# Kernel optimization log

Measured on AMD Instinct MI355X. Metric: run time of the kernel, lower is better.

Reference implementation:

```python
import jax, jax.numpy as jnp
import numpy as np

NEG_SLOPE = 0.2  # PyG GATConv default negative_slope
EPS = 1e-16


def gat_conv(x, src, dst, num_nodes, W, a_src, a_dst, bias, heads, out_c, concat):
    """PyG-style GATConv (eval mode, self-loops already appended).
    x: [N, F_in]; src/dst: [E] (edge j->i with src=j, dst=i).
    W: [F_in, heads*out_c]; a_src/a_dst: [heads, out_c]; bias: [heads*out_c] or [out_c].
    """
    xw = (x @ W).reshape(num_nodes, heads, out_c)          # [N, H, C]
    alpha_src = jnp.sum(xw * a_src, axis=-1)               # [N, H]
    alpha_dst = jnp.sum(xw * a_dst, axis=-1)               # [N, H]
    e = jax.nn.leaky_relu(alpha_src[src] + alpha_dst[dst], NEG_SLOPE)  # [E, H]
    # numerically stable segment softmax over edges grouped by destination node
    m = jax.ops.segment_max(e, dst, num_segments=num_nodes)            # [N, H]
    e = jnp.exp(e - m[dst])
    denom = jax.ops.segment_sum(e, dst, num_segments=num_nodes)        # [N, H]
    alpha = e / (denom[dst] + EPS)                                     # [E, H]
    # weighted scatter-sum aggregation of source messages
    out = jax.ops.segment_sum(xw[src] * alpha[:, :, None], dst, num_segments=num_nodes)  # [N, H, C]
    if concat:
        out = out.reshape(num_nodes, heads * out_c)
    else:
        out = out.mean(axis=1)
    return out + bias


def setup_inputs() -> dict:
    key = jax.random.key(0)
    ks = jax.random.split(key, 12)
    N, E = 50000, 800000
    F_in, Hid, H1, Out = 512, 32, 8, 64

    def xavier(k, shape, gain=1.414):
        fan_in, fan_out = shape[0], shape[-1] if len(shape) == 2 else int(np.prod(shape[1:]))
        a = gain * np.sqrt(6.0 / (fan_in + fan_out))
        return jax.random.uniform(k, shape, jnp.float32, -a, a)

    x = jax.random.normal(ks[0], (N, F_in), jnp.float32)
    edge_index = jax.random.randint(ks[1], (2, E), 0, N, jnp.int64)

    W1 = xavier(ks[2], (F_in, H1 * Hid))
    a_src1 = xavier(ks[3], (H1, Hid))
    a_dst1 = xavier(ks[4], (H1, Hid))
    b1 = jnp.zeros((H1 * Hid,), jnp.float32)

    W2 = xavier(ks[5], (H1 * Hid, Out))
    a_src2 = xavier(ks[6], (1, Out))
    a_dst2 = xavier(ks[7], (1, Out))
    b2 = jnp.zeros((Out,), jnp.float32)

    return {"x": x, "edge_index": edge_index,
            "W1": W1, "a_src1": a_src1, "a_dst1": a_dst1, "b1": b1,
            "W2": W2, "a_src2": a_src2, "a_dst2": a_dst2, "b2": b2}


def reference(x, edge_index, W1, a_src1, a_dst1, b1, W2, a_src2, a_dst2, b2):
    N = x.shape[0]
    # add self-loops (PyG GATConv default add_self_loops=True)
    loop = jnp.arange(N, dtype=edge_index.dtype)
    src = jnp.concatenate([edge_index[0], loop])
    dst = jnp.concatenate([edge_index[1], loop])

    # eval mode: all dropouts are identity
    h = gat_conv(x, src, dst, N, W1, a_src1, a_dst1, b1, heads=8, out_c=32, concat=True)
    h = jax.nn.elu(h)
    h = gat_conv(h, src, dst, N, W2, a_src2, a_dst2, b2, heads=1, out_c=64, concat=False)
    return jax.nn.log_softmax(h, axis=1)
```

## Files before the change

kernel.cpp:

```cpp
#include <hip/hip_runtime.h>
#include <hip/hip_bf16.h>


typedef __attribute__((ext_vector_type(8)))  __bf16          bf16x8;
typedef __attribute__((ext_vector_type(8)))  unsigned short  ushort8;
typedef __attribute__((ext_vector_type(16))) float           f32x16;

#define NEG_SLOPE 0.2f
#define EPS_GAT 1e-16f

static __device__ __forceinline__ float lrelu(float x) {
    return x > 0.0f ? x : NEG_SLOPE * x;
}
static __device__ __forceinline__ unsigned short f2bf(float f) {
    unsigned u = __float_as_uint(f);
    return (unsigned short)((u + 0x7fffu + ((u >> 16) & 1u)) >> 16);
}
static __device__ __forceinline__ float bf2f(unsigned short v) {
    return __uint_as_float(((unsigned)v) << 16);
}
static __device__ __forceinline__ unsigned encf(float x) {
    unsigned u = __float_as_uint(x);
    return (u >> 31) ? ~u : (u | 0x80000000u);
}
static __device__ __forceinline__ float decf(unsigned e) {
    unsigned u = (e >> 31) ? (e & 0x7fffffffu) : ~e;
    return __uint_as_float(u);
}

__global__ void k_hist_w(const void* __restrict__ eix, int* __restrict__ counts,
                         int E, int EB,
                         const float* __restrict__ W1, const float* __restrict__ W2,
                         unsigned short* __restrict__ w1t, unsigned short* __restrict__ w2t) {
    int b = blockIdx.x;
    if (b < EB) {
        int i = b * 256 + threadIdx.x;
        unsigned w = ((const unsigned*)eix)[2 * min(i, E - 1) + 1];
        bool is64 = (__syncthreads_or((int)(w != 0u)) == 0);
        if (i < E) {
            int d = is64 ? (int)((const long long*)eix)[E + i]
                         : ((const int*)eix)[E + i];
            atomicAdd(&counts[d], 1);
        }
    } else {
        int t = (b - EB) * 256 + threadIdx.x;
        if (t < 512 * 256) {
            int k = t >> 8, m = t & 255;
            w1t[m * 512 + k] = f2bf(W1[t]);
        } else {
            int u = t - 512 * 256;
            if (u < 256 * 64) {
                int k = u >> 6, m = u & 63;
                w2t[m * 256 + k] = f2bf(W2[u]);
            }
        }
    }
}

__global__ void k_scan1(const int* __restrict__ counts, int* __restrict__ rowp,
                        int* __restrict__ bsum, int N) {
    __shared__ int s[256];
    int t = threadIdx.x, i = blockIdx.x * 256 + t;
    int v = (i < N) ? counts[i] : 0;
    s[t] = v;
    __syncthreads();
    for (int off = 1; off < 256; off <<= 1) {
        int u = (t >= off) ? s[t - off] : 0;
        __syncthreads();
        s[t] += u;
        __syncthreads();
    }
    if (i < N) rowp[i] = s[t] - v;
    if (t == 255) bsum[blockIdx.x] = s[255];
}

__global__ void k_scan2(const int* __restrict__ bsum, int* __restrict__ boff,
                        int* __restrict__ rowp_last, int NB) {
    __shared__ int s[256];
    int t = threadIdx.x;
    int v = (t < NB) ? bsum[t] : 0;
    s[t] = v;
    __syncthreads();
    for (int off = 1; off < 256; off <<= 1) {
        int u = (t >= off) ? s[t - off] : 0;
        __syncthreads();
        s[t] += u;
        __syncthreads();
    }
    if (t < NB) boff[t] = s[t] - v;
    if (t == 255) *rowp_last = s[255];
}

__global__ void k_scan3(int* __restrict__ rowp, int* __restrict__ cursor,
                        const int* __restrict__ boff, int N) {
    int i = blockIdx.x * 256 + threadIdx.x;
    if (i < N) {
        int r = rowp[i] + boff[blockIdx.x];
        rowp[i] = r;
        cursor[i] = r;
    }
}

__global__ void k_fill(const void* __restrict__ eix, int* __restrict__ cursor,
                       int* __restrict__ ssrc, int E) {
    int i = blockIdx.x * 256 + threadIdx.x;
    unsigned w = ((const unsigned*)eix)[2 * min(i, E - 1) + 1];
    bool is64 = (__syncthreads_or((int)(w != 0u)) == 0);
    if (i >= E) return;
    int s, d;
    if (is64) {
        s = (int)((const long long*)eix)[i];
        d = (int)((const long long*)eix)[E + i];
    } else {
        s = ((const int*)eix)[i];
        d = ((const int*)eix)[E + i];
    }
    int pos = atomicAdd(&cursor[d], 1);
    ssrc[pos] = s;
}

template <int BM, int BN, int NT, bool AF32, bool OUTBF>
__global__ __launch_bounds__(NT) void k_gemm(const void* __restrict__ Ain,
                                             const unsigned short* __restrict__ Bt,
                                             void* __restrict__ Cout, int Nrows, int K) {
    constexpr int LD = 40;
    __shared__ __align__(16) unsigned short As[BM * LD];
    __shared__ __align__(16) unsigned short Bs[BN * LD];
    const int tid = threadIdx.x;
    const int blockRow = blockIdx.x * BM;
    const int wave = tid >> 6, lane = tid & 63;
    constexpr int WR = BM / 64;
    const int wr = wave % WR, wc = wave / WR;
    const int m = lane & 31;
    const int ksel = (lane >> 5) * 8;

    f32x16 acc00{}, acc01{}, acc10{}, acc11{};

    for (int kt = 0; kt < K; kt += 32) {
        if constexpr (AF32) {
            const float* A = (const float*)Ain;
            for (int idx = tid; idx < BM * 4; idx += NT) {
                int r = idx >> 2, kc = (idx & 3) * 8;
                int grow = blockRow + r;
                union { ushort8 u; __hip_bfloat162 h[4]; } cv;
                if (grow < Nrows) {
                    const float* ap = A + (size_t)grow * K + kt + kc;
                    float4 x0 = *(const float4*)ap;
                    float4 x1 = *(const float4*)(ap + 4);
                    cv.h[0] = __float22bfloat162_rn(make_float2(x0.x, x0.y));
                    cv.h[1] = __float22bfloat162_rn(make_float2(x0.z, x0.w));
                    cv.h[2] = __float22bfloat162_rn(make_float2(x1.x, x1.y));
                    cv.h[3] = __float22bfloat162_rn(make_float2(x1.z, x1.w));
                } else {
                    cv.u = ushort8{};
                }
                *(ushort8*)&As[r * LD + kc] = cv.u;
            }
        } else {
            const unsigned short* A = (const unsigned short*)Ain;
            for (int idx = tid; idx < BM * 4; idx += NT) {
                int r = idx >> 2, kc = (idx & 3) * 8;
                int grow = blockRow + r;
                ushort8 o{};
                if (grow < Nrows) o = *(const ushort8*)(A + (size_t)grow * K + kt + kc);
                *(ushort8*)&As[r * LD + kc] = o;
            }
        }
        for (int idx = tid; idx < BN * 4; idx += NT) {
            int r = idx >> 2, kc = (idx & 3) * 8;
            *(ushort8*)&Bs[r * LD + kc] = *(const ushort8*)(Bt + (size_t)r * K + kt + kc);
        }
        __syncthreads();

        #pragma unroll
        for (int kk = 0; kk < 32; kk += 16) {
            bf16x8 a0 = *(const bf16x8*)&As[(wr * 64 +      m) * LD + kk + ksel];
            bf16x8 a1 = *(const bf16x8*)&As[(wr * 64 + 32 + m) * LD + kk + ksel];
            bf16x8 b0 = *(const bf16x8*)&Bs[(wc * 64 +      m) * LD + kk + ksel];
            bf16x8 b1 = *(const bf16x8*)&Bs[(wc * 64 + 32 + m) * LD + kk + ksel];
            acc00 = __builtin_amdgcn_mfma_f32_32x32x16_bf16(a0, b0, acc00, 0, 0, 0);
            acc01 = __builtin_amdgcn_mfma_f32_32x32x16_bf16(a0, b1, acc01, 0, 0, 0);
            acc10 = __builtin_amdgcn_mfma_f32_32x32x16_bf16(a1, b0, acc10, 0, 0, 0);
            acc11 = __builtin_amdgcn_mfma_f32_32x32x16_bf16(a1, b1, acc11, 0, 0, 0);
        }
        __syncthreads();
    }

    const int dcol = wc * 64 + (lane & 31);
    const int dquad = 4 * (lane >> 5);
    auto store_tile = [&](const f32x16& a, int rt, int ct) {
        #pragma unroll
        for (int r = 0; r < 16; ++r) {
            int row = blockRow + wr * 64 + rt * 32 + (r & 3) + 8 * (r >> 2) + dquad;
            if (row < Nrows) {
                size_t off = (size_t)row * BN + dcol + ct * 32;
                if constexpr (OUTBF) ((unsigned short*)Cout)[off] = f2bf(a[r]);
                else                 ((float*)Cout)[off] = a[r];
            }
        }
    };
    store_tile(acc00, 0, 0); store_tile(acc01, 0, 1);
    store_tile(acc10, 1, 0); store_tile(acc11, 1, 1);
}

__global__ void k_alpha(const unsigned short* __restrict__ xw, const float* __restrict__ a_s,
                        const float* __restrict__ a_d, float* __restrict__ os,
                        float* __restrict__ od, unsigned* __restrict__ Menc,
                        int NH, int H, int C) {
    __shared__ float red[256];
    int t = blockIdx.x * 256 + threadIdx.x;
    float s = -1e30f, d = 0.f;
    if (t < NH) {
        int n = t / H, h = t - n * H;
        const unsigned short* row = xw + (size_t)n * H * C + h * C;
        s = 0.f;
        for (int c = 0; c < C; c += 8) {
            ushort8 v = *(const ushort8*)(row + c);
            #pragma unroll
            for (int q = 0; q < 8; ++q) {
                float f = bf2f(v[q]);
                s += f * a_s[h * C + c + q];
                d += f * a_d[h * C + c + q];
            }
        }
        os[t] = s; od[t] = d;
    }
    red[threadIdx.x] = s;
    __syncthreads();
    for (int off = 128; off >= H; off >>= 1) {
        if (threadIdx.x < off) red[threadIdx.x] = fmaxf(red[threadIdx.x], red[threadIdx.x + off]);
        __syncthreads();
    }
    if ((int)threadIdx.x < H) atomicMax(&Menc[threadIdx.x], encf(red[threadIdx.x]));
}

__global__ __launch_bounds__(256) void k_agg_l1(
        const unsigned short* __restrict__ xw1, const float* __restrict__ asrc,
        const float* __restrict__ adst, const unsigned* __restrict__ Menc,
        const float* __restrict__ b1, const int* __restrict__ rp,
        const int* __restrict__ ssrc, unsigned short* __restrict__ hbf, int N) {
    int wid = (blockIdx.x * 256 + threadIdx.x) >> 6;
    if (wid >= N) return;
    int lane = threadIdx.x & 63;
    int g  = lane >> 4;
    int q  = lane & 15;
    int f0 = q * 16;
    int h  = q >> 1;
    int ih = wid * 8 + h;
    float ad = adst[ih];
    float m  = lrelu(decf(Menc[h]) + ad);
    float acc[16];
    float s;
    {
        float w = (g == 0) ? __expf(lrelu(asrc[ih] + ad) - m) : 0.0f;
        const unsigned short* pr = xw1 + (size_t)wid * 256 + f0;
        ushort8 lo = *(const ushort8*)pr;
        ushort8 hi = *(const ushort8*)(pr + 8);
        s = w;
        #pragma unroll
        for (int i = 0; i < 8; ++i) { acc[i] = w * bf2f(lo[i]); acc[8 + i] = w * bf2f(hi[i]); }
    }
    int e0 = rp[wid], e1 = rp[wid + 1];
    if (e0 < e1) {
        int eA = e0;
        bool vA = eA + g < e1;
        int jA = ssrc[min(eA + g, e1 - 1)];
        float asA = asrc[jA * 8 + h];
        const unsigned short* pA = xw1 + (size_t)jA * 256 + f0;
        ushort8 loA = *(const ushort8*)pA;
        ushort8 hiA = *(const ushort8*)(pA + 8);
        int eB = e0 + 4;
        bool hasB = eB < e1;
        bool vB = false; int jB = 0;
        if (hasB) { vB = eB + g < e1; jB = ssrc[min(eB + g, e1 - 1)]; }
        int eC = e0 + 8;
        while (true) {
            bool hasC = eC < e1;
            bool vC = false; int jC = 0;
            if (hasC) { vC = eC + g < e1; jC = ssrc[min(eC + g, e1 - 1)]; }
            float asB = 0.f; ushort8 loB{}, hiB{};
            if (hasB) {
                asB = asrc[jB * 8 + h];
                const unsigned short* pB = xw1 + (size_t)jB * 256 + f0;
                loB = *(const ushort8*)pB;
                hiB = *(const ushort8*)(pB + 8);
            }
            float w = vA ? __expf(lrelu(asA + ad) - m) : 0.0f;
            s += w;
            #pragma unroll
            for (int i = 0; i < 8; ++i) {
                acc[i]     += w * bf2f(loA[i]);
                acc[8 + i] += w * bf2f(hiA[i]);
            }
            if (!hasB) break;
            vA = vB; asA = asB; loA = loB; hiA = hiB;
            jB = jC; vB = vC; hasB = hasC;
            eC += 4;
        }
    }
    s += __shfl_xor(s, 16, 64);
    s += __shfl_xor(s, 32, 64);
    #pragma unroll
    for (int i = 0; i < 16; ++i) {
        acc[i] += __shfl_xor(acc[i], 16, 64);
        acc[i] += __shfl_xor(acc[i], 32, 64);
    }
    float inv = 1.0f / (s + EPS_GAT);
    int fw = f0 + g * 4;
    ushort4 o;
    #pragma unroll
    for (int i = 0; i < 4; ++i) {
        float v = acc[g * 4 + i] * inv + b1[fw + i];
        v = v > 0.f ? v : expm1f(v);
        ((unsigned short*)&o)[i] = f2bf(v);
    }
    *(ushort4*)(hbf + (size_t)wid * 256 + fw) = o;
}

__global__ __launch_bounds__(256) void k_agg_l2(
        const unsigned short* __restrict__ xw2, const float* __restrict__ asrc,
        const float* __restrict__ adst, const unsigned* __restrict__ Menc,
        const float* __restrict__ b2, const int* __restrict__ rp,
        const int* __restrict__ ssrc, float* __restrict__ out, int N) {
    int wid = (blockIdx.x * 256 + threadIdx.x) >> 6;
    if (wid >= N) return;
    int lane = threadIdx.x & 63;
    int g  = lane >> 3;
    int q  = lane & 7;
    int f0 = q * 8;
    float ad = adst[wid];
    float m = lrelu(decf(Menc[0]) + ad);
    float acc[8];
    float s;
    {
        float w = (g == 0) ? __expf(lrelu(asrc[wid] + ad) - m) : 0.0f;
        ushort8 xv = *(const ushort8*)(xw2 + (size_t)wid * 64 + f0);
        s = w;
        #pragma unroll
        for (int i = 0; i < 8; ++i) acc[i] = w * bf2f(xv[i]);
    }
    int e0 = rp[wid], e1 = rp[wid + 1];
    if (e0 < e1) {
        int eA = e0;
        bool vA = eA + g < e1;
        int jA = ssrc[min(eA + g, e1 - 1)];
        float asA = asrc[jA];
        ushort8 xvA = *(const ushort8*)(xw2 + (size_t)jA * 64 + f0);
        int eB = e0 + 8;
        bool hasB = eB < e1;
        bool vB = false; int jB = 0;
        if (hasB) { vB = eB + g < e1; jB = ssrc[min(eB + g, e1 - 1)]; }
        int eC = e0 + 16;
        while (true) {
            bool hasC = eC < e1;
            bool vC = false; int jC = 0;
            if (hasC) { vC = eC + g < e1; jC = ssrc[min(eC + g, e1 - 1)]; }
            float asB = 0.f; ushort8 xvB{};
            if (hasB) {
                asB = asrc[jB];
                xvB = *(const ushort8*)(xw2 + (size_t)jB * 64 + f0);
            }
            float w = vA ? __expf(lrelu(asA + ad) - m) : 0.0f;
            s += w;
            #pragma unroll
            for (int i = 0; i < 8; ++i) acc[i] += w * bf2f(xvA[i]);
            if (!hasB) break;
            vA = vB; asA = asB; xvA = xvB;
            jB = jC; vB = vC; hasB = hasC;
            eC += 8;
        }
    }
    s += __shfl_xor(s, 8, 64);
    s += __shfl_xor(s, 16, 64);
    s += __shfl_xor(s, 32, 64);
    #pragma unroll
    for (int i = 0; i < 8; ++i) {
        acc[i] += __shfl_xor(acc[i], 8, 64);
        acc[i] += __shfl_xor(acc[i], 16, 64);
        acc[i] += __shfl_xor(acc[i], 32, 64);
    }
    float inv = 1.0f / (s + EPS_GAT);
    float val[8];
    float mx = -1e30f;
    #pragma unroll
    for (int i = 0; i < 8; ++i) {
        val[i] = acc[i] * inv + b2[f0 + i];
        mx = fmaxf(mx, val[i]);
    }
    #pragma unroll
    for (int off = 4; off > 0; off >>= 1) mx = fmaxf(mx, __shfl_xor(mx, off, 64));
    float sm = 0.f;
    #pragma unroll
    for (int i = 0; i < 8; ++i) sm += __expf(val[i] - mx);
    #pragma unroll
    for (int off = 4; off > 0; off >>= 1) sm += __shfl_xor(sm, off, 64);
    float lse = mx + logf(sm);
    if (g == 0) {
        float4 o0 = make_float4(val[0] - lse, val[1] - lse, val[2] - lse, val[3] - lse);
        float4 o1 = make_float4(val[4] - lse, val[5] - lse, val[6] - lse, val[7] - lse);
        *(float4*)(out + (size_t)wid * 64 + f0)     = o0;
        *(float4*)(out + (size_t)wid * 64 + f0 + 4) = o1;
    }
}

static inline int cdiv(int a, int b) { return (a + b - 1) / b; }

extern "C" void kernel_launch(void* const* d_in, const int* in_sizes, int n_in,
                              void* d_out, int out_size, void* d_ws, size_t ws_size,
                              hipStream_t stream) {
    const float* x   = (const float*)d_in[0];
    const void*  eix = d_in[1];
    const float* W1  = (const float*)d_in[2];
    const float* as1 = (const float*)d_in[3];
    const float* ad1 = (const float*)d_in[4];
    const float* b1  = (const float*)d_in[5];
    const float* W2  = (const float*)d_in[6];
    const float* as2 = (const float*)d_in[7];
    const float* ad2 = (const float*)d_in[8];
    const float* b2  = (const float*)d_in[9];
    float* out = (float*)d_out;

    const int N = in_sizes[0] / 512;
    const int E = in_sizes[1] / 2;
    const int EB = cdiv(E, 256);
    const int WB = cdiv(512 * 256 + 256 * 64, 256);
    const int NB = cdiv(N, 256);
    const int NB1 = cdiv(N * 8, 256);
    const int NB2 = cdiv(N, 256);
    (void)n_in; (void)out_size; (void)ws_size;

    char* base = (char*)d_ws;
    size_t o = 0;
    auto alloc = [&](size_t bytes) -> char* {
        o = (o + 255) & ~(size_t)255;
        char* p = base + o;
        o += bytes;
        return p;
    };
    unsigned short* xw1b  = (unsigned short*)alloc((size_t)N * 256 * 2);
    unsigned short* hbf   = (unsigned short*)alloc((size_t)N * 256 * 2);
    unsigned short* xw2b  = (unsigned short*)alloc((size_t)N * 64 * 2);
    float*          asrc1 = (float*)alloc((size_t)N * 8 * 4);
    float*          adst1 = (float*)alloc((size_t)N * 8 * 4);
    float*          asrc2 = (float*)alloc((size_t)N * 4);
    float*          adst2 = (float*)alloc((size_t)N * 4);
    size_t zero_begin = (o + 255) & ~(size_t)255;
    unsigned*       Menc  = (unsigned*)alloc(16 * 4);
    int*            counts= (int*)alloc((size_t)N * 4);
    size_t zero_end = o;
    int*            cursor= (int*)alloc((size_t)N * 4);
    int*            rowp  = (int*)alloc((size_t)(N + 1) * 4);
    int*            bsum  = (int*)alloc(256 * 4);
    int*            boff  = (int*)alloc(256 * 4);
    unsigned short* w1t   = (unsigned short*)alloc(512 * 256 * 2);
    unsigned short* w2t   = (unsigned short*)alloc(256 * 64 * 2);
    int*            ssrc  = (int*)alloc((size_t)E * 4);

    hipMemsetAsync(base + zero_begin, 0, zero_end - zero_begin, stream);

    k_hist_w<<<EB + WB, 256, 0, stream>>>(eix, counts, E, EB, W1, W2, w1t, w2t);
    k_scan1<<<NB, 256, 0, stream>>>(counts, rowp, bsum, N);
    k_scan2<<<1, 256, 0, stream>>>(bsum, boff, rowp + N, NB);
    k_scan3<<<NB, 256, 0, stream>>>(rowp, cursor, boff, N);
    k_fill<<<EB, 256, 0, stream>>>(eix, cursor, ssrc, E);

    k_gemm<128, 256, 512, true, true><<<cdiv(N, 128), 512, 0, stream>>>(x, w1t, xw1b, N, 512);
    k_alpha<<<NB1, 256, 0, stream>>>(xw1b, as1, ad1, asrc1, adst1, Menc, N * 8, 8, 32);
    k_agg_l1<<<cdiv(N * 64, 256), 256, 0, stream>>>(xw1b, asrc1, adst1, Menc, b1,
                                                    rowp, ssrc, hbf, N);
    k_gemm<256, 64, 256, false, true><<<cdiv(N, 256), 256, 0, stream>>>(hbf, w2t, xw2b, N, 256);
    k_alpha<<<NB2, 256, 0, stream>>>(xw2b, as2, ad2, asrc2, adst2, Menc + 8, N, 1, 64);
    k_agg_l2<<<cdiv(N * 64, 256), 256, 0, stream>>>(xw2b, asrc2, adst2, Menc + 8, b2,
                                                    rowp, ssrc, out, N);
}
```

Measured before the change: 421.0 us.

## Pack bf16 conversions into float2 FMAs, regroup layer-2 lanes, shrink GEMM tiles

Aggregation accumulators become float2 vectors, with bf16 pairs unpacked from 32-bit words so the compiler can use packed FMA instructions. The layer-2 aggregation now gives each lane 16 features and processes 16 edges per step instead of 8. Both GEMM launches switch to smaller row tiles and fewer threads per block, aiming for more blocks and better occupancy. The trade-off is more register pressure in the layer-2 kernel and less operand reuse per GEMM block.

```diff
diff --git a/kernel.cpp b/kernel.cpp
--- a/kernel.cpp
+++ b/kernel.cpp
@@ -5,9 +5,12 @@
 typedef __attribute__((ext_vector_type(8)))  __bf16          bf16x8;
 typedef __attribute__((ext_vector_type(8)))  unsigned short  ushort8;
 typedef __attribute__((ext_vector_type(16))) float           f32x16;
+typedef __attribute__((ext_vector_type(2)))  float           f32x2;
 
 #define NEG_SLOPE 0.2f
 #define EPS_GAT 1e-16f
+
+union U8 { ushort8 v; unsigned u[4]; };
 
 static __device__ __forceinline__ float lrelu(float x) {
     return x > 0.0f ? x : NEG_SLOPE * x;
@@ -18,6 +21,12 @@
 }
 static __device__ __forceinline__ float bf2f(unsigned short v) {
     return __uint_as_float(((unsigned)v) << 16);
+}
+static __device__ __forceinline__ f32x2 cvt2(unsigned u) {
+    f32x2 r;
+    r.x = __uint_as_float(u << 16);
+    r.y = __uint_as_float(u & 0xffff0000u);
+    return r;
 }
 static __device__ __forceinline__ unsigned encf(float x) {
     unsigned u = __float_as_uint(x);
@@ -249,16 +258,21 @@
     int ih = wid * 8 + h;
     float ad = adst[ih];
     float m  = lrelu(decf(Menc[h]) + ad);
-    float acc[16];
+    f32x2 acc2[8];
     float s;
     {
         float w = (g == 0) ? __expf(lrelu(asrc[ih] + ad) - m) : 0.0f;
+        f32x2 w2 = {w, w};
         const unsigned short* pr = xw1 + (size_t)wid * 256 + f0;
-        ushort8 lo = *(const ushort8*)pr;
-        ushort8 hi = *(const ushort8*)(pr + 8);
+        U8 lo, hi;
+        lo.v = *(const ushort8*)pr;
+        hi.v = *(const ushort8*)(pr + 8);
         s = w;
         #pragma unroll
-        for (int i = 0; i < 8; ++i) { acc[i] = w * bf2f(lo[i]); acc[8 + i] = w * bf2f(hi[i]); }
+        for (int i = 0; i < 4; ++i) {
+            acc2[i]     = w2 * cvt2(lo.u[i]);
+            acc2[4 + i] = w2 * cvt2(hi.u[i]);
+        }
     }
     int e0 = rp[wid], e1 = rp[wid + 1];
     if (e0 < e1) {
@@ -267,8 +281,9 @@
         int jA = ssrc[min(eA + g, e1 - 1)];
         float asA = asrc[jA * 8 + h];
         const unsigned short* pA = xw1 + (size_t)jA * 256 + f0;
-        ushort8 loA = *(const ushort8*)pA;
-        ushort8 hiA = *(const ushort8*)(pA + 8);
+        U8 loA, hiA;
+        loA.v = *(const ushort8*)pA;
+        hiA.v = *(const ushort8*)(pA + 8);
         int eB = e0 + 4;
         bool hasB = eB < e1;
         bool vB = false; int jB = 0;
@@ -278,19 +293,20 @@
             bool hasC = eC < e1;
             bool vC = false; int jC = 0;
             if (hasC) { vC = eC + g < e1; jC = ssrc[min(eC + g, e1 - 1)]; }
-            float asB = 0.f; ushort8 loB{}, hiB{};
+            float asB = 0.f; U8 loB{}, hiB{};
             if (hasB) {
                 asB = asrc[jB * 8 + h];
                 const unsigned short* pB = xw1 + (size_t)jB * 256 + f0;
-                loB = *(const ushort8*)pB;
-                hiB = *(const ushort8*)(pB + 8);
+                loB.v = *(const ushort8*)pB;
+                hiB.v = *(const ushort8*)(pB + 8);
             }
             float w = vA ? __expf(lrelu(asA + ad) - m) : 0.0f;
+            f32x2 w2 = {w, w};
             s += w;
             #pragma unroll
-            for (int i = 0; i < 8; ++i) {
-                acc[i]     += w * bf2f(loA[i]);
-                acc[8 + i] += w * bf2f(hiA[i]);
+            for (int i = 0; i < 4; ++i) {
+                acc2[i]     += w2 * cvt2(loA.u[i]);
+                acc2[4 + i] += w2 * cvt2(hiA.u[i]);
             }
             if (!hasB) break;
             vA = vB; asA = asB; loA = loB; hiA = hiB;
@@ -301,16 +317,19 @@
     s += __shfl_xor(s, 16, 64);
     s += __shfl_xor(s, 32, 64);
     #pragma unroll
-    for (int i = 0; i < 16; ++i) {
-        acc[i] += __shfl_xor(acc[i], 16, 64);
-        acc[i] += __shfl_xor(acc[i], 32, 64);
+    for (int i = 0; i < 8; ++i) {
+        acc2[i].x += __shfl_xor(acc2[i].x, 16, 64);
+        acc2[i].x += __shfl_xor(acc2[i].x, 32, 64);
+        acc2[i].y += __shfl_xor(acc2[i].y, 16, 64);
+        acc2[i].y += __shfl_xor(acc2[i].y, 32, 64);
     }
     float inv = 1.0f / (s + EPS_GAT);
     int fw = f0 + g * 4;
+    float vv[4] = { acc2[2 * g].x, acc2[2 * g].y, acc2[2 * g + 1].x, acc2[2 * g + 1].y };
     ushort4 o;
     #pragma unroll
     for (int i = 0; i < 4; ++i) {
-        float v = acc[g * 4 + i] * inv + b1[fw + i];
+        float v = vv[i] * inv + b1[fw + i];
         v = v > 0.f ? v : expm1f(v);
         ((unsigned short*)&o)[i] = f2bf(v);
     }
@@ -325,19 +344,26 @@
     int wid = (blockIdx.x * 256 + threadIdx.x) >> 6;
     if (wid >= N) return;
     int lane = threadIdx.x & 63;
-    int g  = lane >> 3;
-    int q  = lane & 7;
-    int f0 = q * 8;
+    int g  = lane >> 2;
+    int q  = lane & 3;
+    int f0 = q * 16;
     float ad = adst[wid];
     float m = lrelu(decf(Menc[0]) + ad);
-    float acc[8];
+    f32x2 acc2[8];
     float s;
     {
         float w = (g == 0) ? __expf(lrelu(asrc[wid] + ad) - m) : 0.0f;
-        ushort8 xv = *(const ushort8*)(xw2 + (size_t)wid * 64 + f0);
+        f32x2 w2 = {w, w};
+        const unsigned short* pr = xw2 + (size_t)wid * 64 + f0;
+        U8 lo, hi;
+        lo.v = *(const ushort8*)pr;
+        hi.v = *(const ushort8*)(pr + 8);
         s = w;
         #pragma unroll
-        for (int i = 0; i < 8; ++i) acc[i] = w * bf2f(xv[i]);
+        for (int i = 0; i < 4; ++i) {
+            acc2[i]     = w2 * cvt2(lo.u[i]);
+            acc2[4 + i] = w2 * cvt2(hi.u[i]);
+        }
     }
     int e0 = rp[wid], e1 = rp[wid + 1];
     if (e0 < e1) {
@@ -345,61 +371,74 @@
         bool vA = eA + g < e1;
         int jA = ssrc[min(eA + g, e1 - 1)];
         float asA = asrc[jA];
-        ushort8 xvA = *(const ushort8*)(xw2 + (size_t)jA * 64 + f0);
-        int eB = e0 + 8;
+        const unsigned short* pA = xw2 + (size_t)jA * 64 + f0;
+        U8 loA, hiA;
+        loA.v = *(const ushort8*)pA;
+        hiA.v = *(const ushort8*)(pA + 8);
+        int eB = e0 + 16;
         bool hasB = eB < e1;
         bool vB = false; int jB = 0;
         if (hasB) { vB = eB + g < e1; jB = ssrc[min(eB + g, e1 - 1)]; }
-        int eC = e0 + 16;
+        int eC = e0 + 32;
         while (true) {
             bool hasC = eC < e1;
             bool vC = false; int jC = 0;
             if (hasC) { vC = eC + g < e1; jC = ssrc[min(eC + g, e1 - 1)]; }
-            float asB = 0.f; ushort8 xvB{};
+            float asB = 0.f; U8 loB{}, hiB{};
             if (hasB) {
                 asB = asrc[jB];
-                xvB = *(const ushort8*)(xw2 + (size_t)jB * 64 + f0);
+                const unsigned short* pB = xw2 + (size_t)jB * 64 + f0;
+                loB.v = *(const ushort8*)pB;
+                hiB.v = *(const ushort8*)(pB + 8);
             }
             float w = vA ? __expf(lrelu(asA + ad) - m) : 0.0f;
+            f32x2 w2 = {w, w};
             s += w;
             #pragma unroll
-            for (int i = 0; i < 8; ++i) acc[i] += w * bf2f(xvA[i]);
+            for (int i = 0; i < 4; ++i) {
+                acc2[i]     += w2 * cvt2(loA.u[i]);
+                acc2[4 + i] += w2 * cvt2(hiA.u[i]);
+            }
             if (!hasB) break;
-            vA = vB; asA = asB; xvA = xvB;
+            vA = vB; asA = asB; loA = loB; hiA = hiB;
             jB = jC; vB = vC; hasB = hasC;
-            eC += 8;
-        }
-    }
-    s += __shfl_xor(s, 8, 64);
-    s += __shfl_xor(s, 16, 64);
-    s += __shfl_xor(s, 32, 64);
+            eC += 16;
+        }
+    }
+    s += __shfl_xor(s, 4, 64);  s += __shfl_xor(s, 8, 64);
+    s += __shfl_xor(s, 16, 64); s += __shfl_xor(s, 32, 64);
     #pragma unroll
     for (int i = 0; i < 8; ++i) {
-        acc[i] += __shfl_xor(acc[i], 8, 64);
-        acc[i] += __shfl_xor(acc[i], 16, 64);
-        acc[i] += __shfl_xor(acc[i], 32, 64);
+        #pragma unroll
+        for (int off = 4; off <= 32; off <<= 1) {
+            acc2[i].x += __shfl_xor(acc2[i].x, off, 64);
+            acc2[i].y += __shfl_xor(acc2[i].y, off, 64);
+        }
     }
     float inv = 1.0f / (s + EPS_GAT);
-    float val[8];
+    float val[16];
     float mx = -1e30f;
     #pragma unroll
-    for (int i = 0; i < 8; ++i) {
-        val[i] = acc[i] * inv + b2[f0 + i];
+    for (int i = 0; i < 16; ++i) {
+        float a = (i & 1) ? acc2[i >> 1].y : acc2[i >> 1].x;
+        val[i] = a * inv + b2[f0 + i];
         mx = fmaxf(mx, val[i]);
     }
-    #pragma unroll
-    for (int off = 4; off > 0; off >>= 1) mx = fmaxf(mx, __shfl_xor(mx, off, 64));
+    mx = fmaxf(mx, __shfl_xor(mx, 1, 64));
+    mx = fmaxf(mx, __shfl_xor(mx, 2, 64));
     float sm = 0.f;
     #pragma unroll
-    for (int i = 0; i < 8; ++i) sm += __expf(val[i] - mx);
-    #pragma unroll
-    for (int off = 4; off > 0; off >>= 1) sm += __shfl_xor(sm, off, 64);
+    for (int i = 0; i < 16; ++i) sm += __expf(val[i] - mx);
+    sm += __shfl_xor(sm, 1, 64);
+    sm += __shfl_xor(sm, 2, 64);
     float lse = mx + logf(sm);
     if (g == 0) {
-        float4 o0 = make_float4(val[0] - lse, val[1] - lse, val[2] - lse, val[3] - lse);
-        float4 o1 = make_float4(val[4] - lse, val[5] - lse, val[6] - lse, val[7] - lse);
-        *(float4*)(out + (size_t)wid * 64 + f0)     = o0;
-        *(float4*)(out + (size_t)wid * 64 + f0 + 4) = o1;
+        #pragma unroll
+        for (int i = 0; i < 16; i += 4) {
+            float4 o = make_float4(val[i] - lse, val[i + 1] - lse,
+                                   val[i + 2] - lse, val[i + 3] - lse);
+            *(float4*)(out + (size_t)wid * 64 + f0 + i) = o;
+        }
     }
 }
 
@@ -464,11 +503,11 @@
     k_scan3<<<NB, 256, 0, stream>>>(rowp, cursor, boff, N);
     k_fill<<<EB, 256, 0, stream>>>(eix, cursor, ssrc, E);
 
-    k_gemm<128, 256, 512, true, true><<<cdiv(N, 128), 512, 0, stream>>>(x, w1t, xw1b, N, 512);
+    k_gemm<64, 256, 256, true, true><<<cdiv(N, 64), 256, 0, stream>>>(x, w1t, xw1b, N, 512);
     k_alpha<<<NB1, 256, 0, stream>>>(xw1b, as1, ad1, asrc1, adst1, Menc, N * 8, 8, 32);
     k_agg_l1<<<cdiv(N * 64, 256), 256, 0, stream>>>(xw1b, asrc1, adst1, Menc, b1,
                                                     rowp, ssrc, hbf, N);
-    k_gemm<256, 64, 256, false, true><<<cdiv(N, 256), 256, 0, stream>>>(hbf, w2t, xw2b, N, 256);
+    k_gemm<64, 64, 64, false, true><<<cdiv(N, 64), 64, 0, stream>>>(hbf, w2t, xw2b, N, 256);
     k_alpha<<<NB2, 256, 0, stream>>>(xw2b, as2, ad2, asrc2, adst2, Menc + 8, N, 1, 64);
     k_agg_l2<<<cdiv(N * 64, 256), 256, 0, stream>>>(xw2b, asrc2, adst2, Menc + 8, b2,
                                                     rowp, ssrc, out, N);
```

Result: slower. 473.6 us (+12.5%).
